# Optimization experiments

Hardware: AMD Instinct MI355X
Metric: run time of the kernel (lower is better)

Reference implementation:

```python
import jax, jax.numpy as jnp
import numpy as np

N = 50000       # original graph nodes (= number of subgraphs, one per node)
S = 10          # nodes per subgraph
M = N * S       # combined subgraph nodes
E = 2_000_000   # combined subgraph edges
E0 = 1_000_000  # original edges
NIN, HOP, NOUT, L = 64, 16, 128, 3
D = NIN + HOP   # conv width (80)


def setup_inputs() -> dict:
    key = jax.random.key(0)
    ks = iter(jax.random.split(key, 40))
    rng = np.random.default_rng(0)

    # structured index tensors: subgraph b occupies rows [b*S, (b+1)*S); row b*S is the centroid
    sub_batch = np.repeat(np.arange(N, dtype=np.int64), S)
    nodes_mapper = rng.integers(0, N, size=M, dtype=np.int64)
    nodes_mapper[::S] = np.arange(N)           # centroid: mapper == batch id
    hop_indicator = rng.integers(1, 5, size=M).astype(np.int64)
    hop_indicator[::S] = 0                     # centroid is hop 0
    edge_index = rng.integers(0, M, size=(2, E), dtype=np.int64)
    edges_mapper = rng.integers(0, E0, size=E, dtype=np.int64)

    def lin(k, fin, fout):
        return jax.random.normal(k, (fin, fout), jnp.float32) / np.sqrt(fin)

    inp = dict(
        x=jax.random.normal(next(ks), (N, NIN), jnp.float32),
        edge_attr=jax.random.normal(next(ks), (E0, D), jnp.float32),
        hop_table=jax.random.normal(next(ks), (20, HOP), jnp.float32),
        conv_W=jax.random.normal(next(ks), (L, D, D), jnp.float32) / np.sqrt(D),
        bn_g=jnp.ones((L, D), jnp.float32),
        bn_b=jnp.zeros((L, D), jnp.float32),
        oe_W0=lin(next(ks), D, NOUT), oe_b0=jnp.zeros((NOUT,), jnp.float32),
        oe_W1=lin(next(ks), NOUT, NOUT), oe_b1=jnp.zeros((NOUT,), jnp.float32),
        oe_W2=lin(next(ks), NOUT, NOUT), oe_b2=jnp.zeros((NOUT,), jnp.float32),
        st_W0=lin(next(ks), NOUT, NOUT), st_b0=jnp.zeros((NOUT,), jnp.float32),
        st_W1=lin(next(ks), NOUT, NOUT), st_b1=jnp.zeros((NOUT,), jnp.float32),
        st_W2=lin(next(ks), NOUT, NOUT), st_b2=jnp.zeros((NOUT,), jnp.float32),
        ct_W0=lin(next(ks), NOUT, NOUT), ct_b0=jnp.zeros((NOUT,), jnp.float32),
        ct_W1=lin(next(ks), NOUT, NOUT), ct_b1=jnp.zeros((NOUT,), jnp.float32),
        ct_W2=lin(next(ks), NOUT, NOUT), ct_b2=jnp.zeros((NOUT,), jnp.float32),
        gc_W=lin(next(ks), HOP, NOUT), gc_b=jnp.zeros((NOUT,), jnp.float32),
        gs_W=lin(next(ks), HOP, NOUT), gs_b=jnp.zeros((NOUT,), jnp.float32),
        gx_W=lin(next(ks), HOP, NOUT), gx_b=jnp.zeros((NOUT,), jnp.float32),
        nodes_mapper=jnp.asarray(nodes_mapper),
        edge_index=jnp.asarray(edge_index),
        edges_mapper=jnp.asarray(edges_mapper),
        sub_batch=jnp.asarray(sub_batch),
        hop_indicator=jnp.asarray(hop_indicator),
    )
    return inp


def _mlp3(h, W0, b0, W1, b1, W2, b2, final_act):
    h = jax.nn.relu(h @ W0 + b0)
    h = jax.nn.relu(h @ W1 + b1)
    h = h @ W2 + b2
    return jax.nn.relu(h) if final_act else h


def reference(x, edge_attr, hop_table, conv_W, bn_g, bn_b,
              oe_W0, oe_b0, oe_W1, oe_b1, oe_W2, oe_b2,
              st_W0, st_b0, st_W1, st_b1, st_W2, st_b2,
              ct_W0, ct_b0, ct_W1, ct_b1, ct_W2, ct_b2,
              gc_W, gc_b, gs_W, gs_b, gx_W, gx_b,
              nodes_mapper, edge_index, edges_mapper, sub_batch, hop_indicator):
    src, dst = edge_index[0], edge_index[1]
    ea = edge_attr[edges_mapper]                              # [E, D] gather
    hemb = hop_table[hop_indicator + 1]                       # [M, HOP]
    h = jnp.concatenate([x[nodes_mapper], hemb], axis=-1)     # [M, D]

    # GNN: nlayer x (GINE-style conv -> relu -> batchnorm(batch stats) -> residual)
    for l in range(L):
        msg = h[src] + ea                                     # [E, D]
        agg = jax.ops.segment_sum(msg, dst, num_segments=M)   # scatter-add
        h2 = jax.nn.relu(agg @ conv_W[l])
        mu = jnp.mean(h2, axis=0)
        var = jnp.var(h2, axis=0)
        h2 = (h2 - mu) * jax.lax.rsqrt(var + 1e-5) * bn_g[l] + bn_b[l]
        h = h2 + h                                            # residual

    # output encoder MLP (no final activation)
    h = _mlp3(h, oe_W0, oe_b0, oe_W1, oe_b1, oe_W2, oe_b2, False)  # [M, NOUT]

    # three views with sigmoid hop gates
    g_c = jax.nn.sigmoid(hemb @ gc_W + gc_b)
    g_s = jax.nn.sigmoid(hemb @ gs_W + gs_b)
    g_x = jax.nn.sigmoid(hemb @ gx_W + gx_b)

    cm = (nodes_mapper == sub_batch)[:, None]                 # centroid mask (one per subgraph)
    centroid_x = jax.ops.segment_sum(jnp.where(cm, h * g_c, 0.0), sub_batch, num_segments=N)
    subgraph_x = jax.ops.segment_sum(
        _mlp3(h, st_W0, st_b0, st_W1, st_b1, st_W2, st_b2, True) * g_s, sub_batch, num_segments=N)
    context_x = jax.ops.segment_sum(
        _mlp3(h, ct_W0, ct_b0, ct_W1, ct_b1, ct_W2, ct_b2, True) * g_x, nodes_mapper, num_segments=N)

    return centroid_x + subgraph_x + context_x                # embs_combine_mode='add'
```

## Files before the change

### kernel.cpp

```cpp
#include <hip/hip_runtime.h>


typedef __attribute__((ext_vector_type(8))) short bf16x8;
typedef __attribute__((ext_vector_type(4))) float f32x4;

static constexpr int cN = 50000;
static constexpr int cM = 500000;
static constexpr int cE = 2000000;

__device__ __forceinline__ float b2f(unsigned short u) {
  union { unsigned int u; float f; } v; v.u = ((unsigned int)u) << 16; return v.f;
}
__device__ __forceinline__ unsigned short f2b(float f) {
  union { float f; unsigned int u; } v; v.f = f;
  unsigned int x = v.u;
  x += 0x7fffu + ((x >> 16) & 1u);
  return (unsigned short)(x >> 16);
}
__device__ __forceinline__ float sigm(float x) { return 1.0f / (1.0f + __expf(-x)); }
__device__ __forceinline__ f32x4 mfma16(bf16x8 a, bf16x8 b, f32x4 c) {
  return __builtin_amdgcn_mfma_f32_16x16x32_bf16(a, b, c, 0, 0, 0);
}

struct RepackDesc { const float* src; unsigned short* dst; int K; int N; int tiles; };
struct RepackArgs { RepackDesc d[15]; };

__global__ __launch_bounds__(256) void repack_kernel(RepackArgs a) {
  RepackDesc dd = a.d[blockIdx.y];
  int tile = blockIdx.x;
  if (tile >= dd.tiles) return;
  int ncb = dd.N >> 4;
  int c = tile / ncb, cb = tile - c * ncb;
  for (int e = threadIdx.x; e < 512; e += 256) {
    int lane = e >> 3, j = e & 7;
    int k = 32 * c + 8 * (lane >> 4) + j;
    int n = 16 * cb + (lane & 15);
    unsigned short v = (k < dd.K) ? f2b(dd.src[(size_t)k * dd.N + n]) : (unsigned short)0;
    dd.dst[(size_t)tile * 512 + e] = v;
  }
}

__global__ __launch_bounds__(256) void build_h_kernel(
    const float* __restrict__ x, const float* __restrict__ ht,
    const int* __restrict__ nmap, const int* __restrict__ hop,
    unsigned short* __restrict__ h)
{
  int i = blockIdx.x * 256 + threadIdx.x;
  if (i >= cM * 20) return;
  int row = i / 20, cc = i - row * 20;
  int col = cc * 4;
  float4 f;
  if (col < 64) {
    f = *(const float4*)(x + (size_t)nmap[row] * 64 + col);
  } else {
    int hi = hop[row] + 1;
    f = *(const float4*)(ht + (size_t)hi * 16 + (col - 64));
  }
  ushort4 o; o.x = f2b(f.x); o.y = f2b(f.y); o.z = f2b(f.z); o.w = f2b(f.w);
  *(ushort4*)(h + (size_t)row * 80 + col) = o;
}

__global__ __launch_bounds__(256) void hist_kernel(const int* __restrict__ ei, int* __restrict__ deg) {
  int e = blockIdx.x * 256 + threadIdx.x;
  if (e < cE) atomicAdd(&deg[ei[cE + e]], 1);
}

__global__ __launch_bounds__(256) void scan1_kernel(const int* __restrict__ deg, int* __restrict__ bsum) {
  __shared__ int s[256];
  int i = blockIdx.x * 256 + threadIdx.x;
  s[threadIdx.x] = (i < cM) ? deg[i] : 0;
  __syncthreads();
  for (int o = 128; o > 0; o >>= 1) {
    if (threadIdx.x < o) s[threadIdx.x] += s[threadIdx.x + o];
    __syncthreads();
  }
  if (threadIdx.x == 0) bsum[blockIdx.x] = s[0];
}

__global__ void scan2_kernel(int* __restrict__ bsum, int nb) {
  if (threadIdx.x == 0 && blockIdx.x == 0) {
    int acc = 0;
    for (int i = 0; i < nb; ++i) { int t = bsum[i]; bsum[i] = acc; acc += t; }
  }
}

__global__ __launch_bounds__(256) void scan3_kernel(
    const int* __restrict__ deg, const int* __restrict__ bsum,
    int* __restrict__ rowptr, int* __restrict__ cursor)
{
  __shared__ int s[256];
  int i = blockIdx.x * 256 + threadIdx.x;
  int v = (i < cM) ? deg[i] : 0;
  s[threadIdx.x] = v;
  __syncthreads();
  for (int o = 1; o < 256; o <<= 1) {
    int t = (threadIdx.x >= o) ? s[threadIdx.x - o] : 0;
    __syncthreads();
    s[threadIdx.x] += t;
    __syncthreads();
  }
  if (i < cM) {
    int ex = bsum[blockIdx.x] + s[threadIdx.x] - v;
    rowptr[i] = ex; cursor[i] = ex;
  }
  if (i == cM - 1) rowptr[cM] = bsum[blockIdx.x] + s[threadIdx.x];
}

__global__ __launch_bounds__(256) void scatter_kernel(
    const int* __restrict__ ei, const int* __restrict__ emap,
    int* __restrict__ cursor, int* __restrict__ srcs, int* __restrict__ em2)
{
  int e = blockIdx.x * 256 + threadIdx.x;
  if (e >= cE) return;
  int d = ei[cE + e];
  int pos = atomicAdd(&cursor[d], 1);
  srcs[pos] = ei[e];
  em2[pos] = emap[e];
}

__global__ __launch_bounds__(320) void eag_rowsum_kernel(
    const float* __restrict__ ea, const int* __restrict__ em2,
    const int* __restrict__ rowptr, unsigned short* __restrict__ eag)
{
  int t = threadIdx.x;
  int r = blockIdx.x * 16 + t / 20;
  int c = (t % 20) * 4;
  if (r >= cM) return;
  int p0 = rowptr[r], p1 = rowptr[r + 1];
  float4 acc = {0.f, 0.f, 0.f, 0.f};
  for (int p = p0; p < p1; ++p) {
    int em = em2[p];
    float4 v = *(const float4*)(ea + (size_t)em * 80 + c);
    acc.x += v.x; acc.y += v.y; acc.z += v.z; acc.w += v.w;
  }
  ushort4 o = {f2b(acc.x), f2b(acc.y), f2b(acc.z), f2b(acc.w)};
  *(ushort4*)(eag + (size_t)r * 80 + c) = o;
}

__global__ __launch_bounds__(320) void aggregate_kernel(
    const unsigned short* __restrict__ h, const unsigned short* __restrict__ eag,
    const int* __restrict__ rowptr, const int* __restrict__ srcs,
    unsigned short* __restrict__ Bo)
{
  int t = threadIdx.x;
  int r = blockIdx.x * 16 + t / 20;
  int c = (t % 20) * 4;
  if (r >= cM) return;
  int p0 = rowptr[r], p1 = rowptr[r + 1];
  ushort4 a0 = *(const ushort4*)(eag + (size_t)r * 80 + c);
  float4 acc = {b2f(a0.x), b2f(a0.y), b2f(a0.z), b2f(a0.w)};
  for (int p = p0; p < p1; ++p) {
    int s = srcs[p];
    ushort4 v = *(const ushort4*)(h + (size_t)s * 80 + c);
    acc.x += b2f(v.x); acc.y += b2f(v.y); acc.z += b2f(v.z); acc.w += b2f(v.w);
  }
  ushort4 o = {f2b(acc.x), f2b(acc.y), f2b(acc.z), f2b(acc.w)};
  *(ushort4*)(Bo + (size_t)r * 80 + c) = o;
}

__global__ __launch_bounds__(256) void edge_scatter_kernel(
    const unsigned short* __restrict__ h, const float* __restrict__ ea,
    const int* __restrict__ ei, const int* __restrict__ emap,
    float* __restrict__ agg)
{
  int i = blockIdx.x * 256 + threadIdx.x;
  if (i >= cE * 20) return;
  int e = i / 20, q = i - e * 20;
  int src = ei[e], dst = ei[cE + e], em = emap[e];
  ushort4 hv = *(const ushort4*)(h + (size_t)src * 80 + q * 4);
  float4 ev = *(const float4*)(ea + (size_t)em * 80 + q * 4);
  float* ap = agg + (size_t)dst * 80 + q * 4;
  atomicAdd(ap + 0, b2f(hv.x) + ev.x);
  atomicAdd(ap + 1, b2f(hv.y) + ev.y);
  atomicAdd(ap + 2, b2f(hv.z) + ev.z);
  atomicAdd(ap + 3, b2f(hv.w) + ev.w);
}

template<bool F32IO>
__global__ __launch_bounds__(256) void conv_gemm_kernel(
    void* __restrict__ aggv, const unsigned short* __restrict__ Bp)
{
  __shared__ __align__(16) unsigned short Bl[7680];
  for (int i = threadIdx.x; i < 7680; i += 256) Bl[i] = Bp[i];
  __syncthreads();
  int lane = threadIdx.x & 63, wave = threadIdx.x >> 6;
  int tile = blockIdx.x * 4 + wave;
  bool act = tile < (cM / 16);
  int quad = lane >> 4, m = lane & 15;
  size_t rowA = (size_t)tile * 16 + m;

  bf16x8 a[3];
  #pragma unroll
  for (int c = 0; c < 3; ++c) {
    bf16x8 av = {0, 0, 0, 0, 0, 0, 0, 0};
    int k = 32 * c + 8 * quad;
    if (act && k + 8 <= 80) {
      if constexpr (F32IO) {
        const float* p = (const float*)aggv + rowA * 80 + k;
        float4 f0 = *(const float4*)p;
        float4 f1 = *(const float4*)(p + 4);
        av[0] = (short)f2b(f0.x); av[1] = (short)f2b(f0.y);
        av[2] = (short)f2b(f0.z); av[3] = (short)f2b(f0.w);
        av[4] = (short)f2b(f1.x); av[5] = (short)f2b(f1.y);
        av[6] = (short)f2b(f1.z); av[7] = (short)f2b(f1.w);
      } else {
        av = *(const bf16x8*)((const unsigned short*)aggv + rowA * 80 + k);
      }
    }
    a[c] = av;
  }

  #pragma unroll
  for (int cb = 0; cb < 5; ++cb) {
    f32x4 acc = {0.f, 0.f, 0.f, 0.f};
    #pragma unroll
    for (int c = 0; c < 3; ++c)
      acc = mfma16(a[c], *(const bf16x8*)(Bl + ((size_t)(c * 5 + cb) * 64 + lane) * 8), acc);
    int col = cb * 16 + m;
    #pragma unroll
    for (int i2 = 0; i2 < 4; ++i2) {
      size_t row = (size_t)tile * 16 + quad * 4 + i2;
      if (act) {
        float v = fmaxf(acc[i2], 0.0f);
        if constexpr (F32IO) ((float*)aggv)[row * 80 + col] = v;
        else ((unsigned short*)aggv)[row * 80 + col] = f2b(v);
      }
    }
  }
}

template<bool F32IO>
__global__ __launch_bounds__(256) void stats_kernel(
    const void* __restrict__ h2v, float* __restrict__ stats)
{
  __shared__ __align__(16) float ssum[12 * 80];
  __shared__ __align__(16) float ssq[12 * 80];
  int t = threadIdx.x;
  int cc = t % 20, slot = t / 20;
  if (slot < 12) {
    float s0 = 0, s1 = 0, s2 = 0, s3 = 0, q0 = 0, q1 = 0, q2 = 0, q3 = 0;
    for (int row = blockIdx.x * 12 + slot; row < cM; row += gridDim.x * 12) {
      float f0, f1, f2, f3;
      if constexpr (F32IO) {
        float4 v = *(const float4*)((const float*)h2v + (size_t)row * 80 + cc * 4);
        f0 = v.x; f1 = v.y; f2 = v.z; f3 = v.w;
      } else {
        ushort4 v = *(const ushort4*)((const unsigned short*)h2v + (size_t)row * 80 + cc * 4);
        f0 = b2f(v.x); f1 = b2f(v.y); f2 = b2f(v.z); f3 = b2f(v.w);
      }
      s0 += f0; s1 += f1; s2 += f2; s3 += f3;
      q0 += f0 * f0; q1 += f1 * f1; q2 += f2 * f2; q3 += f3 * f3;
    }
    int base = slot * 80 + cc * 4;
    ssum[base + 0] = s0; ssum[base + 1] = s1; ssum[base + 2] = s2; ssum[base + 3] = s3;
    ssq[base + 0] = q0; ssq[base + 1] = q1; ssq[base + 2] = q2; ssq[base + 3] = q3;
  }
  __syncthreads();
  if (t < 20) {
    for (int j = 0; j < 4; ++j) {
      int c = t * 4 + j;
      float s = 0, q = 0;
      for (int sl = 0; sl < 12; ++sl) { s += ssum[sl * 80 + c]; q += ssq[sl * 80 + c]; }
      atomicAdd(&stats[c], s);
      atomicAdd(&stats[80 + c], q);
    }
  }
}

template<bool F32IO>
__global__ __launch_bounds__(256) void bn_residual_kernel(
    const void* __restrict__ h2v, const float* __restrict__ stats,
    const float* __restrict__ g, const float* __restrict__ b,
    unsigned short* __restrict__ h)
{
  int i = blockIdx.x * 256 + threadIdx.x;
  if (i >= cM * 20) return;
  int row = i / 20, cc = i - row * 20;
  int col = cc * 4;
  float in2[4];
  if constexpr (F32IO) {
    float4 v2 = *(const float4*)((const float*)h2v + (size_t)row * 80 + col);
    in2[0] = v2.x; in2[1] = v2.y; in2[2] = v2.z; in2[3] = v2.w;
  } else {
    ushort4 v2 = *(const ushort4*)((const unsigned short*)h2v + (size_t)row * 80 + col);
    in2[0] = b2f(v2.x); in2[1] = b2f(v2.y); in2[2] = b2f(v2.z); in2[3] = b2f(v2.w);
  }
  ushort4 vh = *(const ushort4*)(h + (size_t)row * 80 + col);
  const float invM = 1.0f / (float)cM;
  unsigned short inh[4] = {vh.x, vh.y, vh.z, vh.w};
  unsigned short o[4];
  #pragma unroll
  for (int j = 0; j < 4; ++j) {
    int c = col + j;
    float mu = stats[c] * invM;
    float var = fmaxf(stats[80 + c] * invM - mu * mu, 0.0f);
    float inv = rsqrtf(var + 1e-5f);
    float val = (in2[j] - mu) * inv * g[c] + b[c] + b2f(inh[j]);
    o[j] = f2b(val);
  }
  ushort4 ov = {o[0], o[1], o[2], o[3]};
  *(ushort4*)(h + (size_t)row * 80 + col) = ov;
}

template<int KCH>
__device__ __forceinline__ void layer_to_tb(
    const bf16x8* a, const unsigned short* Wl, const float* biasl,
    unsigned short* tbw, int lane)
{
  int quad = lane >> 4, m = lane & 15;
  #pragma unroll
  for (int cb = 0; cb < 8; ++cb) {
    f32x4 acc = {0.f, 0.f, 0.f, 0.f};
    #pragma unroll
    for (int c = 0; c < KCH; ++c)
      acc = mfma16(a[c], *(const bf16x8*)(Wl + ((size_t)(c * 8 + cb) * 64 + lane) * 8), acc);
    int col = cb * 16 + m;
    float bv = biasl[col];
    #pragma unroll
    for (int i2 = 0; i2 < 4; ++i2)
      tbw[(quad * 4 + i2) * 136 + col] = f2b(fmaxf(acc[i2] + bv, 0.0f));
  }
}

__device__ __forceinline__ void tb_to_a(bf16x8* a, const unsigned short* tbw, int lane) {
  int quad = lane >> 4, m = lane & 15;
  #pragma unroll
  for (int c = 0; c < 4; ++c)
    a[c] = *(const bf16x8*)(tbw + m * 136 + 32 * c + 8 * quad);
}

__device__ __forceinline__ bf16x8 load_hemb(const float* ht, int hi, int quad) {
  bf16x8 he = {0, 0, 0, 0, 0, 0, 0, 0};
  if (quad < 2) {
    const float* p = ht + (size_t)hi * 16 + 8 * quad;
    float4 f0 = *(const float4*)p;
    float4 f1 = *(const float4*)(p + 4);
    he[0] = (short)f2b(f0.x); he[1] = (short)f2b(f0.y);
    he[2] = (short)f2b(f0.z); he[3] = (short)f2b(f0.w);
    he[4] = (short)f2b(f1.x); he[5] = (short)f2b(f1.y);
    he[6] = (short)f2b(f1.z); he[7] = (short)f2b(f1.w);
  }
  return he;
}

__global__ __launch_bounds__(256) void oe_fused_kernel(
    const unsigned short* __restrict__ h,
    const unsigned short* __restrict__ P0, const float* __restrict__ b0,
    const unsigned short* __restrict__ P1, const float* __restrict__ b1,
    const unsigned short* __restrict__ P2, const float* __restrict__ b2,
    unsigned short* __restrict__ Out)
{
  __shared__ __align__(16) unsigned short Wbuf[16384];
  __shared__ __align__(16) float bias[3][128];
  __shared__ __align__(16) unsigned short tb[4][16 * 136];
  int t = threadIdx.x;
  for (int i = t; i < 12288; i += 256) Wbuf[i] = P0[i];
  if (t < 128) { bias[0][t] = b0[t]; bias[1][t] = b1[t]; bias[2][t] = b2[t]; }
  __syncthreads();

  int lane = t & 63, wave = t >> 6;
  int tile = blockIdx.x * 4 + wave;
  bool act = tile < (cM / 16);
  int quad = lane >> 4, m = lane & 15;
  size_t rowA = (size_t)tile * 16 + m;

  bf16x8 a[4];
  #pragma unroll
  for (int c = 0; c < 4; ++c) {
    bf16x8 av = {0, 0, 0, 0, 0, 0, 0, 0};
    int k = 32 * c + 8 * quad;
    if (act && c < 3 && k + 8 <= 80)
      av = *(const bf16x8*)(h + rowA * 80 + k);
    a[c] = av;
  }
  layer_to_tb<3>(a, Wbuf, bias[0], tb[wave], lane);
  __syncthreads();
  tb_to_a(a, tb[wave], lane);
  for (int i = t; i < 16384; i += 256) Wbuf[i] = P1[i];
  __syncthreads();
  layer_to_tb<4>(a, Wbuf, bias[1], tb[wave], lane);
  __syncthreads();
  tb_to_a(a, tb[wave], lane);
  for (int i = t; i < 16384; i += 256) Wbuf[i] = P2[i];
  __syncthreads();

  #pragma unroll
  for (int cb = 0; cb < 8; ++cb) {
    f32x4 acc = {0.f, 0.f, 0.f, 0.f};
    #pragma unroll
    for (int c = 0; c < 4; ++c)
      acc = mfma16(a[c], *(const bf16x8*)(Wbuf + ((size_t)(c * 8 + cb) * 64 + lane) * 8), acc);
    int col = cb * 16 + m;
    float bv = bias[2][col];
    #pragma unroll
    for (int i2 = 0; i2 < 4; ++i2) {
      size_t row = (size_t)tile * 16 + quad * 4 + i2;
      if (act) Out[row * 128 + col] = f2b(acc[i2] + bv);
    }
  }
}

__global__ __launch_bounds__(256) void st_fused_kernel(
    const unsigned short* __restrict__ hout,
    const unsigned short* __restrict__ P0, const float* __restrict__ b0,
    const unsigned short* __restrict__ P1, const float* __restrict__ b1,
    const unsigned short* __restrict__ P2, const float* __restrict__ b2,
    const unsigned short* __restrict__ Gs, const float* __restrict__ gsb,
    const unsigned short* __restrict__ Gc, const float* __restrict__ gcb,
    const float* __restrict__ ht, const int* __restrict__ hop,
    const int* __restrict__ nmap, const int* __restrict__ sb,
    float* __restrict__ outp)
{
  __shared__ __align__(16) unsigned short Wbuf[16384];
  __shared__ __align__(16) float bias[5][128];
  __shared__ __align__(16) unsigned short tb[4][16 * 136];
  int t = threadIdx.x;
  for (int i = t; i < 16384; i += 256) Wbuf[i] = P0[i];
  if (t < 128) {
    bias[0][t] = b0[t]; bias[1][t] = b1[t]; bias[2][t] = b2[t];
    bias[3][t] = gsb[t]; bias[4][t] = gcb[t];
  }
  __syncthreads();

  int lane = t & 63, wave = t >> 6;
  int tile = blockIdx.x * 4 + wave;
  bool act = tile < (cM / 16);
  int quad = lane >> 4, m = lane & 15;
  size_t rowA = (size_t)tile * 16 + m;

  bf16x8 a[4];
  #pragma unroll
  for (int c = 0; c < 4; ++c) {
    bf16x8 av = {0, 0, 0, 0, 0, 0, 0, 0};
    if (act) av = *(const bf16x8*)(hout + rowA * 128 + 32 * c + 8 * quad);
    a[c] = av;
  }
  layer_to_tb<4>(a, Wbuf, bias[0], tb[wave], lane);
  __syncthreads();
  tb_to_a(a, tb[wave], lane);
  for (int i = t; i < 16384; i += 256) Wbuf[i] = P1[i];
  __syncthreads();
  layer_to_tb<4>(a, Wbuf, bias[1], tb[wave], lane);
  __syncthreads();
  tb_to_a(a, tb[wave], lane);
  for (int i = t; i < 16384; i += 256) Wbuf[i] = P2[i];
  __syncthreads();
  float* red = (float*)&tb[0][0];
  for (int i = t; i < 1024; i += 256) red[i] = 0.0f;
  int sbBase = sb[blockIdx.x * 64];
  __syncthreads();

  int hi = act ? (hop[rowA] + 1) : 0;
  bf16x8 he = load_hemb(ht, hi, quad);

  int r[4], sbr[4]; bool mk[4];
  #pragma unroll
  for (int i2 = 0; i2 < 4; ++i2) {
    int row = tile * 16 + quad * 4 + i2;
    r[i2] = row;
    sbr[i2] = act ? sb[row] : 0;
    mk[i2] = act && (nmap[row] == sbr[i2]);
  }

  #pragma unroll
  for (int cb = 0; cb < 8; ++cb) {
    f32x4 acc = {0.f, 0.f, 0.f, 0.f}, ga = {0.f, 0.f, 0.f, 0.f}, ca = {0.f, 0.f, 0.f, 0.f};
    #pragma unroll
    for (int c = 0; c < 4; ++c)
      acc = mfma16(a[c], *(const bf16x8*)(Wbuf + ((size_t)(c * 8 + cb) * 64 + lane) * 8), acc);
    ga = mfma16(he, *(const bf16x8*)(Gs + ((size_t)cb * 64 + lane) * 8), ga);
    ca = mfma16(he, *(const bf16x8*)(Gc + ((size_t)cb * 64 + lane) * 8), ca);
    int col = cb * 16 + m;
    #pragma unroll
    for (int i2 = 0; i2 < 4; ++i2) {
      float v = fmaxf(acc[i2] + bias[2][col], 0.0f) * sigm(ga[i2] + bias[3][col]);
      if (mk[i2]) v += b2f(hout[(size_t)r[i2] * 128 + col]) * sigm(ca[i2] + bias[4][col]);
      if (act) {
        int slot = sbr[i2] - sbBase;
        if ((unsigned)slot < 8u) atomicAdd(&red[slot * 128 + col], v);
        else atomicAdd(outp + (size_t)sbr[i2] * 128 + col, v);
      }
    }
  }

  __syncthreads();
  for (int i = t; i < 1024; i += 256) {
    float v = red[i];
    if (v != 0.0f)
      atomicAdd(outp + (size_t)(sbBase + (i >> 7)) * 128 + (i & 127), v);
  }
}

__global__ __launch_bounds__(256) void ct_fused_kernel(
    const unsigned short* __restrict__ hout,
    const unsigned short* __restrict__ P0, const float* __restrict__ b0,
    const unsigned short* __restrict__ P1, const float* __restrict__ b1,
    const unsigned short* __restrict__ P2, const float* __restrict__ b2,
    const unsigned short* __restrict__ Gx, const float* __restrict__ gxb,
    const float* __restrict__ ht, const int* __restrict__ hop,
    const int* __restrict__ nmap,
    float* __restrict__ outp)
{
  __shared__ __align__(16) unsigned short Wbuf[16384];
  __shared__ __align__(16) float bias[4][128];
  __shared__ __align__(16) unsigned short tb[4][16 * 136];
  int t = threadIdx.x;
  for (int i = t; i < 16384; i += 256) Wbuf[i] = P0[i];
  if (t < 128) {
    bias[0][t] = b0[t]; bias[1][t] = b1[t];
    bias[2][t] = b2[t]; bias[3][t] = gxb[t];
  }
  __syncthreads();

  int lane = t & 63, wave = t >> 6;
  int tile = blockIdx.x * 4 + wave;
  bool act = tile < (cM / 16);
  int quad = lane >> 4, m = lane & 15;
  size_t rowA = (size_t)tile * 16 + m;

  bf16x8 a[4];
  #pragma unroll
  for (int c = 0; c < 4; ++c) {
    bf16x8 av = {0, 0, 0, 0, 0, 0, 0, 0};
    if (act) av = *(const bf16x8*)(hout + rowA * 128 + 32 * c + 8 * quad);
    a[c] = av;
  }
  layer_to_tb<4>(a, Wbuf, bias[0], tb[wave], lane);
  __syncthreads();
  tb_to_a(a, tb[wave], lane);
  for (int i = t; i < 16384; i += 256) Wbuf[i] = P1[i];
  __syncthreads();
  layer_to_tb<4>(a, Wbuf, bias[1], tb[wave], lane);
  __syncthreads();
  tb_to_a(a, tb[wave], lane);
  for (int i = t; i < 16384; i += 256) Wbuf[i] = P2[i];
  __syncthreads();

  int hi = act ? (hop[rowA] + 1) : 0;
  bf16x8 he = load_hemb(ht, hi, quad);

  int dst[4];
  #pragma unroll
  for (int i2 = 0; i2 < 4; ++i2) {
    int row = tile * 16 + quad * 4 + i2;
    dst[i2] = act ? nmap[row] : 0;
  }

  #pragma unroll
  for (int cb = 0; cb < 8; ++cb) {
    f32x4 acc = {0.f, 0.f, 0.f, 0.f}, ga = {0.f, 0.f, 0.f, 0.f};
    #pragma unroll
    for (int c = 0; c < 4; ++c)
      acc = mfma16(a[c], *(const bf16x8*)(Wbuf + ((size_t)(c * 8 + cb) * 64 + lane) * 8), acc);
    ga = mfma16(he, *(const bf16x8*)(Gx + ((size_t)cb * 64 + lane) * 8), ga);
    int col = cb * 16 + m;
    #pragma unroll
    for (int i2 = 0; i2 < 4; ++i2) {
      float v = fmaxf(acc[i2] + bias[2][col], 0.0f) * sigm(ga[i2] + bias[3][col]);
      if (act) atomicAdd(outp + (size_t)dst[i2] * 128 + col, v);
    }
  }
}

extern "C" void kernel_launch(void* const* d_in, const int* in_sizes, int n_in,
                              void* d_out, int out_size, void* d_ws, size_t ws_size,
                              hipStream_t stream)
{
  const float* x     = (const float*)d_in[0];
  const float* eattr = (const float*)d_in[1];
  const float* htab  = (const float*)d_in[2];
  const float* convW = (const float*)d_in[3];
  const float* bng   = (const float*)d_in[4];
  const float* bnb   = (const float*)d_in[5];
  const float* oeW0 = (const float*)d_in[6];  const float* oeb0 = (const float*)d_in[7];
  const float* oeW1 = (const float*)d_in[8];  const float* oeb1 = (const float*)d_in[9];
  const float* oeW2 = (const float*)d_in[10]; const float* oeb2 = (const float*)d_in[11];
  const float* stW0 = (const float*)d_in[12]; const float* stb0 = (const float*)d_in[13];
  const float* stW1 = (const float*)d_in[14]; const float* stb1 = (const float*)d_in[15];
  const float* stW2 = (const float*)d_in[16]; const float* stb2 = (const float*)d_in[17];
  const float* ctW0 = (const float*)d_in[18]; const float* ctb0 = (const float*)d_in[19];
  const float* ctW1 = (const float*)d_in[20]; const float* ctb1 = (const float*)d_in[21];
  const float* ctW2 = (const float*)d_in[22]; const float* ctb2 = (const float*)d_in[23];
  const float* gcW = (const float*)d_in[24]; const float* gcb = (const float*)d_in[25];
  const float* gsW = (const float*)d_in[26]; const float* gsb = (const float*)d_in[27];
  const float* gxW = (const float*)d_in[28]; const float* gxb = (const float*)d_in[29];
  const int* nmap = (const int*)d_in[30];
  const int* ei   = (const int*)d_in[31];
  const int* emap = (const int*)d_in[32];
  const int* sb   = (const int*)d_in[33];
  const int* hop  = (const int*)d_in[34];

  if (n_in < 35 ||
      in_sizes[0] != cN * 64 || in_sizes[1] != 1000000 * 80 ||
      in_sizes[2] != 20 * 16 || in_sizes[3] != 3 * 80 * 80 ||
      in_sizes[30] != cM || in_sizes[31] != 2 * cE || in_sizes[32] != cE ||
      in_sizes[33] != cM || in_sizes[34] != cM || out_size != cN * 128)
    return;

  const size_t PCONV0 = 0, PCONV1 = 7680, PCONV2 = 15360, POE0 = 23040,
               POE1 = 35328, POE2 = 51712, PST0 = 68096, PST1 = 84480,
               PST2 = 100864, PCT0 = 117248, PCT1 = 133632, PCT2 = 150016,
               PGC = 166400, PGS = 170496, PGX = 174592;
  const size_t PACK_BYTES = 178688 * 2 + 256;

  char* ws = (char*)d_ws;
  size_t off = 0;
  auto alloc = [&](size_t bytes) -> void* {
    void* p = ws + off; off += (bytes + 255) & ~(size_t)255; return p;
  };

  unsigned short* h    = (unsigned short*)alloc((size_t)cM * 80 * 2);
  unsigned short* Aeag = (unsigned short*)alloc((size_t)cM * 80 * 2);
  unsigned short* Bagg = (unsigned short*)alloc((size_t)cM * 80 * 2);
  int*   rowptr = (int*)alloc((size_t)(cM + 1) * 4);
  int*   srcs   = (int*)alloc((size_t)cE * 4);
  float* stats  = (float*)alloc(1024);
  unsigned short* packs = (unsigned short*)alloc(PACK_BYTES);
  size_t needFast = off;
  bool fast = (ws_size >= needFast);

  float* aggF = nullptr;
  if (!fast) {
    off = 0;
    h     = (unsigned short*)alloc((size_t)cM * 80 * 2);
    aggF  = (float*)alloc((size_t)cM * 80 * 4);
    stats = (float*)alloc(1024);
    packs = (unsigned short*)alloc(PACK_BYTES);
    if (ws_size < off) return;
  }

  RepackArgs ra;
  auto setd = [&](int idx, const float* src, size_t dstOff, int K, int Nn, int tiles) {
    ra.d[idx].src = src; ra.d[idx].dst = packs + dstOff;
    ra.d[idx].K = K; ra.d[idx].N = Nn; ra.d[idx].tiles = tiles;
  };
  setd(0, convW,          PCONV0, 80, 80, 15);
  setd(1, convW + 6400,   PCONV1, 80, 80, 15);
  setd(2, convW + 12800,  PCONV2, 80, 80, 15);
  setd(3, oeW0, POE0, 80, 128, 24);
  setd(4, oeW1, POE1, 128, 128, 32);
  setd(5, oeW2, POE2, 128, 128, 32);
  setd(6, stW0, PST0, 128, 128, 32);
  setd(7, stW1, PST1, 128, 128, 32);
  setd(8, stW2, PST2, 128, 128, 32);
  setd(9, ctW0, PCT0, 128, 128, 32);
  setd(10, ctW1, PCT1, 128, 128, 32);
  setd(11, ctW2, PCT2, 128, 128, 32);
  setd(12, gcW, PGC, 16, 128, 8);
  setd(13, gsW, PGS, 16, 128, 8);
  setd(14, gxW, PGX, 16, 128, 8);
  repack_kernel<<<dim3(32, 15), 256, 0, stream>>>(ra);

  const int elemBlocksM = (cM * 20 + 255) / 256;
  const int gemmBlocks  = (cM / 16 + 3) / 4;
  const int rowBlocks   = (cM + 15) / 16;
  const int edgeB256    = (cE + 255) / 256;
  const int scanBlocks  = (cM + 255) / 256;

  build_h_kernel<<<elemBlocksM, 256, 0, stream>>>(x, htab, nmap, hop, h);
  hipMemsetAsync(d_out, 0, (size_t)cN * 128 * 4, stream);

  unsigned short* hout;

  if (fast) {
    int* deg    = (int*)Bagg;
    int* cursor = deg + cM;
    int* em2    = cursor + cM;
    int* bsum   = em2 + cE;

    hipMemsetAsync(deg, 0, (size_t)cM * 4, stream);
    hist_kernel<<<edgeB256, 256, 0, stream>>>(ei, deg);
    scan1_kernel<<<scanBlocks, 256, 0, stream>>>(deg, bsum);
    scan2_kernel<<<1, 64, 0, stream>>>(bsum, scanBlocks);
    scan3_kernel<<<scanBlocks, 256, 0, stream>>>(deg, bsum, rowptr, cursor);
    scatter_kernel<<<edgeB256, 256, 0, stream>>>(ei, emap, cursor, srcs, em2);
    eag_rowsum_kernel<<<rowBlocks, 320, 0, stream>>>(eattr, em2, rowptr, Aeag);

    for (int l = 0; l < 3; ++l) {
      aggregate_kernel<<<rowBlocks, 320, 0, stream>>>(h, Aeag, rowptr, srcs, Bagg);
      conv_gemm_kernel<false><<<gemmBlocks, 256, 0, stream>>>(
          Bagg, packs + (l == 0 ? PCONV0 : l == 1 ? PCONV1 : PCONV2));
      hipMemsetAsync(stats, 0, 160 * 4, stream);
      stats_kernel<false><<<1024, 256, 0, stream>>>(Bagg, stats);
      bn_residual_kernel<false><<<elemBlocksM, 256, 0, stream>>>(
          Bagg, stats, bng + l * 80, bnb + l * 80, h);
    }
    hout = Aeag;
  } else {
    const int edgeBlocks = (cE * 20) / 256;
    for (int l = 0; l < 3; ++l) {
      hipMemsetAsync(aggF, 0, (size_t)cM * 80 * 4, stream);
      edge_scatter_kernel<<<edgeBlocks, 256, 0, stream>>>(h, eattr, ei, emap, aggF);
      conv_gemm_kernel<true><<<gemmBlocks, 256, 0, stream>>>(
          aggF, packs + (l == 0 ? PCONV0 : l == 1 ? PCONV1 : PCONV2));
      hipMemsetAsync(stats, 0, 160 * 4, stream);
      stats_kernel<true><<<1024, 256, 0, stream>>>(aggF, stats);
      bn_residual_kernel<true><<<elemBlocksM, 256, 0, stream>>>(
          aggF, stats, bng + l * 80, bnb + l * 80, h);
    }
    hout = (unsigned short*)aggF;
  }

  oe_fused_kernel<<<gemmBlocks, 256, 0, stream>>>(
      h, packs + POE0, oeb0, packs + POE1, oeb1, packs + POE2, oeb2, hout);

  st_fused_kernel<<<gemmBlocks, 256, 0, stream>>>(
      hout, packs + PST0, stb0, packs + PST1, stb1, packs + PST2, stb2,
      packs + PGS, gsb, packs + PGC, gcb, htab, hop, nmap, sb, (float*)d_out);

  ct_fused_kernel<<<gemmBlocks, 256, 0, stream>>>(
      hout, packs + PCT0, ctb0, packs + PCT1, ctb1, packs + PCT2, ctb2,
      packs + PGX, gxb, htab, hop, nmap, (float*)d_out);
}
```

Measured before the change: 2.920 ms.

## Fuse output-encoder and view MLPs into one kernel with precomputed gate table

Merges the three tail kernels (output encoder, subgraph MLP, context MLP) into a single kernel that keeps the encoder output in registers and shared memory, so the [M,128] bf16 intermediate is never written to or re-read from global memory. Sigmoid hop gates depend only on the 20-entry hop table, so they are precomputed once into a small gate table instead of being evaluated per row with extra MFMAs and exponentials. The conv GEMM now handles four tiles per wave and stages weights with 16-byte copies, and the shared-memory staging buffer is XOR-swizzled instead of padded. In exchange the fused kernel has higher register and shared-memory pressure and restages weights many times per block, which may lower occupancy.

New measurement: 2.823 ms. -3.3%, faster.

```diff
diff --git a/kernel.cpp b/kernel.cpp
--- a/kernel.cpp
+++ b/kernel.cpp
@@ -7,6 +7,12 @@
 static constexpr int cN = 50000;
 static constexpr int cM = 500000;
 static constexpr int cE = 2000000;
+static constexpr int cTiles = cM / 16;
+
+static constexpr size_t PCONV0 = 0, PCONV1 = 7680, PCONV2 = 15360, POE0 = 23040,
+                        POE1 = 35328, POE2 = 51712, PST0 = 68096, PST1 = 84480,
+                        PST2 = 100864, PCT0 = 117248, PCT1 = 133632, PCT2 = 150016;
+static constexpr size_t PACK_BYTES = 166400 * 2 + 256;
 
 __device__ __forceinline__ float b2f(unsigned short u) {
   union { unsigned int u; float f; } v; v.u = ((unsigned int)u) << 16; return v.f;
@@ -23,7 +29,7 @@
 }
 
 struct RepackDesc { const float* src; unsigned short* dst; int K; int N; int tiles; };
-struct RepackArgs { RepackDesc d[15]; };
+struct RepackArgs { RepackDesc d[12]; };
 
 __global__ __launch_bounds__(256) void repack_kernel(RepackArgs a) {
   RepackDesc dd = a.d[blockIdx.y];
@@ -40,6 +46,25 @@
   }
 }
 
+__global__ __launch_bounds__(256) void gate_build_kernel(
+    const float* __restrict__ ht,
+    const float* __restrict__ gsW, const float* __restrict__ gsb,
+    const float* __restrict__ gcW, const float* __restrict__ gcb,
+    const float* __restrict__ gxW, const float* __restrict__ gxb,
+    float* __restrict__ gtab)
+{
+  int i = blockIdx.x * 256 + threadIdx.x;
+  if (i >= 3 * 20 * 128) return;
+  int g = i / 2560, rem = i - g * 2560;
+  int hi = rem >> 7, col = rem & 127;
+  const float* W  = (g == 0) ? gsW : (g == 1) ? gcW : gxW;
+  const float* bb = (g == 0) ? gsb : (g == 1) ? gcb : gxb;
+  float acc = bb[col];
+  #pragma unroll
+  for (int k = 0; k < 16; ++k) acc += ht[hi * 16 + k] * W[k * 128 + col];
+  gtab[i] = sigm(acc);
+}
+
 __global__ __launch_bounds__(256) void build_h_kernel(
     const float* __restrict__ x, const float* __restrict__ ht,
     const int* __restrict__ nmap, const int* __restrict__ hop,
@@ -181,49 +206,60 @@
     void* __restrict__ aggv, const unsigned short* __restrict__ Bp)
 {
   __shared__ __align__(16) unsigned short Bl[7680];
-  for (int i = threadIdx.x; i < 7680; i += 256) Bl[i] = Bp[i];
+  #pragma unroll
+  for (int i = threadIdx.x; i < 960; i += 256)
+    ((uint4*)Bl)[i] = ((const uint4*)Bp)[i];
   __syncthreads();
   int lane = threadIdx.x & 63, wave = threadIdx.x >> 6;
-  int tile = blockIdx.x * 4 + wave;
-  bool act = tile < (cM / 16);
+  int tile0 = (blockIdx.x * 4 + wave) * 4;
   int quad = lane >> 4, m = lane & 15;
-  size_t rowA = (size_t)tile * 16 + m;
-
-  bf16x8 a[3];
-  #pragma unroll
-  for (int c = 0; c < 3; ++c) {
-    bf16x8 av = {0, 0, 0, 0, 0, 0, 0, 0};
-    int k = 32 * c + 8 * quad;
-    if (act && k + 8 <= 80) {
-      if constexpr (F32IO) {
-        const float* p = (const float*)aggv + rowA * 80 + k;
-        float4 f0 = *(const float4*)p;
-        float4 f1 = *(const float4*)(p + 4);
-        av[0] = (short)f2b(f0.x); av[1] = (short)f2b(f0.y);
-        av[2] = (short)f2b(f0.z); av[3] = (short)f2b(f0.w);
-        av[4] = (short)f2b(f1.x); av[5] = (short)f2b(f1.y);
-        av[6] = (short)f2b(f1.z); av[7] = (short)f2b(f1.w);
-      } else {
-        av = *(const bf16x8*)((const unsigned short*)aggv + rowA * 80 + k);
+
+  bf16x8 a[4][3];
+  #pragma unroll
+  for (int tt = 0; tt < 4; ++tt) {
+    int tile = tile0 + tt;
+    bool act = tile < cTiles;
+    size_t rowA = (size_t)tile * 16 + m;
+    #pragma unroll
+    for (int c = 0; c < 3; ++c) {
+      bf16x8 av = {0, 0, 0, 0, 0, 0, 0, 0};
+      int k = 32 * c + 8 * quad;
+      if (act && k + 8 <= 80) {
+        if constexpr (F32IO) {
+          const float* p = (const float*)aggv + rowA * 80 + k;
+          float4 f0 = *(const float4*)p;
+          float4 f1 = *(const float4*)(p + 4);
+          av[0] = (short)f2b(f0.x); av[1] = (short)f2b(f0.y);
+          av[2] = (short)f2b(f0.z); av[3] = (short)f2b(f0.w);
+          av[4] = (short)f2b(f1.x); av[5] = (short)f2b(f1.y);
+          av[6] = (short)f2b(f1.z); av[7] = (short)f2b(f1.w);
+        } else {
+          av = *(const bf16x8*)((const unsigned short*)aggv + rowA * 80 + k);
+        }
       }
-    }
-    a[c] = av;
-  }
-
-  #pragma unroll
-  for (int cb = 0; cb < 5; ++cb) {
-    f32x4 acc = {0.f, 0.f, 0.f, 0.f};
-    #pragma unroll
-    for (int c = 0; c < 3; ++c)
-      acc = mfma16(a[c], *(const bf16x8*)(Bl + ((size_t)(c * 5 + cb) * 64 + lane) * 8), acc);
-    int col = cb * 16 + m;
-    #pragma unroll
-    for (int i2 = 0; i2 < 4; ++i2) {
-      size_t row = (size_t)tile * 16 + quad * 4 + i2;
-      if (act) {
-        float v = fmaxf(acc[i2], 0.0f);
-        if constexpr (F32IO) ((float*)aggv)[row * 80 + col] = v;
-        else ((unsigned short*)aggv)[row * 80 + col] = f2b(v);
+      a[tt][c] = av;
+    }
+  }
+
+  #pragma unroll
+  for (int tt = 0; tt < 4; ++tt) {
+    int tile = tile0 + tt;
+    bool act = tile < cTiles;
+    #pragma unroll
+    for (int cb = 0; cb < 5; ++cb) {
+      f32x4 acc = {0.f, 0.f, 0.f, 0.f};
+      #pragma unroll
+      for (int c = 0; c < 3; ++c)
+        acc = mfma16(a[tt][c], *(const bf16x8*)(Bl + ((size_t)(c * 5 + cb) * 64 + lane) * 8), acc);
+      int col = cb * 16 + m;
+      #pragma unroll
+      for (int i2 = 0; i2 < 4; ++i2) {
+        size_t row = (size_t)tile * 16 + quad * 4 + i2;
+        if (act) {
+          float v = fmaxf(acc[i2], 0.0f);
+          if constexpr (F32IO) ((float*)aggv)[row * 80 + col] = v;
+          else ((unsigned short*)aggv)[row * 80 + col] = f2b(v);
+        }
       }
     }
   }
@@ -302,9 +338,23 @@
   *(ushort4*)(h + (size_t)row * 80 + col) = ov;
 }
 
+__device__ __forceinline__ void tb_put(unsigned short* tbw, int row, int col, unsigned short v) {
+  int g = (col >> 3) ^ (row & 7);
+  tbw[row * 128 + (g << 3) + (col & 7)] = v;
+}
+
+__device__ __forceinline__ void tb_to_a(bf16x8* a, const unsigned short* tbw, int lane) {
+  int quad = lane >> 4, m = lane & 15;
+  #pragma unroll
+  for (int c = 0; c < 4; ++c) {
+    int sg = ((c << 2) | quad) ^ (m & 7);
+    a[c] = *(const bf16x8*)(tbw + m * 128 + (sg << 3));
+  }
+}
+
 template<int KCH>
-__device__ __forceinline__ void layer_to_tb(
-    const bf16x8* a, const unsigned short* Wl, const float* biasl,
+__device__ __forceinline__ void layer_relu(
+    const bf16x8* a, const unsigned short* Wl, const float* bl,
     unsigned short* tbw, int lane)
 {
   int quad = lane >> 4, m = lane & 15;
@@ -315,166 +365,129 @@
     for (int c = 0; c < KCH; ++c)
       acc = mfma16(a[c], *(const bf16x8*)(Wl + ((size_t)(c * 8 + cb) * 64 + lane) * 8), acc);
     int col = cb * 16 + m;
-    float bv = biasl[col];
+    float bv = bl[col];
     #pragma unroll
     for (int i2 = 0; i2 < 4; ++i2)
-      tbw[(quad * 4 + i2) * 136 + col] = f2b(fmaxf(acc[i2] + bv, 0.0f));
-  }
-}
-
-__device__ __forceinline__ void tb_to_a(bf16x8* a, const unsigned short* tbw, int lane) {
-  int quad = lane >> 4, m = lane & 15;
-  #pragma unroll
-  for (int c = 0; c < 4; ++c)
-    a[c] = *(const bf16x8*)(tbw + m * 136 + 32 * c + 8 * quad);
-}
-
-__device__ __forceinline__ bf16x8 load_hemb(const float* ht, int hi, int quad) {
-  bf16x8 he = {0, 0, 0, 0, 0, 0, 0, 0};
-  if (quad < 2) {
-    const float* p = ht + (size_t)hi * 16 + 8 * quad;
-    float4 f0 = *(const float4*)p;
-    float4 f1 = *(const float4*)(p + 4);
-    he[0] = (short)f2b(f0.x); he[1] = (short)f2b(f0.y);
-    he[2] = (short)f2b(f0.z); he[3] = (short)f2b(f0.w);
-    he[4] = (short)f2b(f1.x); he[5] = (short)f2b(f1.y);
-    he[6] = (short)f2b(f1.z); he[7] = (short)f2b(f1.w);
-  }
-  return he;
-}
-
-__global__ __launch_bounds__(256) void oe_fused_kernel(
+      tb_put(tbw, quad * 4 + i2, col, f2b(fmaxf(acc[i2] + bv, 0.0f)));
+  }
+}
+
+__device__ __forceinline__ void stageW(unsigned short* Wbuf, const unsigned short* src, int nU4, int t) {
+  const uint4* s = (const uint4*)src;
+  uint4* d = (uint4*)Wbuf;
+  for (int i = t; i < nU4; i += 256) d[i] = s[i];
+}
+
+__global__ __launch_bounds__(256, 3) void tail_fused_kernel(
     const unsigned short* __restrict__ h,
-    const unsigned short* __restrict__ P0, const float* __restrict__ b0,
-    const unsigned short* __restrict__ P1, const float* __restrict__ b1,
-    const unsigned short* __restrict__ P2, const float* __restrict__ b2,
-    unsigned short* __restrict__ Out)
+    const unsigned short* __restrict__ packs,
+    const float* __restrict__ oeb0, const float* __restrict__ oeb1, const float* __restrict__ oeb2,
+    const float* __restrict__ stb0, const float* __restrict__ stb1, const float* __restrict__ stb2,
+    const float* __restrict__ ctb0, const float* __restrict__ ctb1, const float* __restrict__ ctb2,
+    const float* __restrict__ gtab,
+    const int* __restrict__ hop, const int* __restrict__ nmap, const int* __restrict__ sb,
+    float* __restrict__ outp)
 {
   __shared__ __align__(16) unsigned short Wbuf[16384];
-  __shared__ __align__(16) float bias[3][128];
-  __shared__ __align__(16) unsigned short tb[4][16 * 136];
+  __shared__ __align__(16) unsigned short tb[4][2048];
+  __shared__ __align__(16) float biasl[9][128];
+
   int t = threadIdx.x;
-  for (int i = t; i < 12288; i += 256) Wbuf[i] = P0[i];
-  if (t < 128) { bias[0][t] = b0[t]; bias[1][t] = b1[t]; bias[2][t] = b2[t]; }
+  stageW(Wbuf, packs + POE0, 1536, t);
+  if (t < 128) {
+    biasl[0][t] = oeb0[t]; biasl[1][t] = oeb1[t]; biasl[2][t] = oeb2[t];
+    biasl[3][t] = stb0[t]; biasl[4][t] = stb1[t]; biasl[5][t] = stb2[t];
+    biasl[6][t] = ctb0[t]; biasl[7][t] = ctb1[t]; biasl[8][t] = ctb2[t];
+  }
   __syncthreads();
 
   int lane = t & 63, wave = t >> 6;
   int tile = blockIdx.x * 4 + wave;
-  bool act = tile < (cM / 16);
+  bool act = tile < cTiles;
   int quad = lane >> 4, m = lane & 15;
   size_t rowA = (size_t)tile * 16 + m;
 
-  bf16x8 a[4];
+  bf16x8 aw[4];
   #pragma unroll
   for (int c = 0; c < 4; ++c) {
     bf16x8 av = {0, 0, 0, 0, 0, 0, 0, 0};
     int k = 32 * c + 8 * quad;
     if (act && c < 3 && k + 8 <= 80)
       av = *(const bf16x8*)(h + rowA * 80 + k);
-    a[c] = av;
-  }
-  layer_to_tb<3>(a, Wbuf, bias[0], tb[wave], lane);
-  __syncthreads();
-  tb_to_a(a, tb[wave], lane);
-  for (int i = t; i < 16384; i += 256) Wbuf[i] = P1[i];
-  __syncthreads();
-  layer_to_tb<4>(a, Wbuf, bias[1], tb[wave], lane);
-  __syncthreads();
-  tb_to_a(a, tb[wave], lane);
-  for (int i = t; i < 16384; i += 256) Wbuf[i] = P2[i];
-  __syncthreads();
-
-  #pragma unroll
-  for (int cb = 0; cb < 8; ++cb) {
-    f32x4 acc = {0.f, 0.f, 0.f, 0.f};
-    #pragma unroll
-    for (int c = 0; c < 4; ++c)
-      acc = mfma16(a[c], *(const bf16x8*)(Wbuf + ((size_t)(c * 8 + cb) * 64 + lane) * 8), acc);
-    int col = cb * 16 + m;
-    float bv = bias[2][col];
-    #pragma unroll
-    for (int i2 = 0; i2 < 4; ++i2) {
-      size_t row = (size_t)tile * 16 + quad * 4 + i2;
-      if (act) Out[row * 128 + col] = f2b(acc[i2] + bv);
-    }
-  }
-}
-
-__global__ __launch_bounds__(256) void st_fused_kernel(
-    const unsigned short* __restrict__ hout,
-    const unsigned short* __restrict__ P0, const float* __restrict__ b0,
-    const unsigned short* __restrict__ P1, const float* __restrict__ b1,
-    const unsigned short* __restrict__ P2, const float* __restrict__ b2,
-    const unsigned short* __restrict__ Gs, const float* __restrict__ gsb,
-    const unsigned short* __restrict__ Gc, const float* __restrict__ gcb,
-    const float* __restrict__ ht, const int* __restrict__ hop,
-    const int* __restrict__ nmap, const int* __restrict__ sb,
-    float* __restrict__ outp)
-{
-  __shared__ __align__(16) unsigned short Wbuf[16384];
-  __shared__ __align__(16) float bias[5][128];
-  __shared__ __align__(16) unsigned short tb[4][16 * 136];
-  int t = threadIdx.x;
-  for (int i = t; i < 16384; i += 256) Wbuf[i] = P0[i];
-  if (t < 128) {
-    bias[0][t] = b0[t]; bias[1][t] = b1[t]; bias[2][t] = b2[t];
-    bias[3][t] = gsb[t]; bias[4][t] = gcb[t];
-  }
-  __syncthreads();
-
-  int lane = t & 63, wave = t >> 6;
-  int tile = blockIdx.x * 4 + wave;
-  bool act = tile < (cM / 16);
-  int quad = lane >> 4, m = lane & 15;
-  size_t rowA = (size_t)tile * 16 + m;
-
-  bf16x8 a[4];
-  #pragma unroll
-  for (int c = 0; c < 4; ++c) {
-    bf16x8 av = {0, 0, 0, 0, 0, 0, 0, 0};
-    if (act) av = *(const bf16x8*)(hout + rowA * 128 + 32 * c + 8 * quad);
-    a[c] = av;
-  }
-  layer_to_tb<4>(a, Wbuf, bias[0], tb[wave], lane);
-  __syncthreads();
-  tb_to_a(a, tb[wave], lane);
-  for (int i = t; i < 16384; i += 256) Wbuf[i] = P1[i];
-  __syncthreads();
-  layer_to_tb<4>(a, Wbuf, bias[1], tb[wave], lane);
-  __syncthreads();
-  tb_to_a(a, tb[wave], lane);
-  for (int i = t; i < 16384; i += 256) Wbuf[i] = P2[i];
-  __syncthreads();
+    aw[c] = av;
+  }
+
+  layer_relu<3>(aw, Wbuf, biasl[0], tb[wave], lane);
+  tb_to_a(aw, tb[wave], lane);
+  __syncthreads();
+  stageW(Wbuf, packs + POE1, 2048, t);
+  __syncthreads();
+  layer_relu<4>(aw, Wbuf, biasl[1], tb[wave], lane);
+  tb_to_a(aw, tb[wave], lane);
+  __syncthreads();
+  stageW(Wbuf, packs + POE2, 2048, t);
+  __syncthreads();
+
+  float o_out[8][4];
+  bf16x8 a_oe[4];
+  {
+    #pragma unroll
+    for (int cb = 0; cb < 8; ++cb) {
+      f32x4 acc = {0.f, 0.f, 0.f, 0.f};
+      #pragma unroll
+      for (int c = 0; c < 4; ++c)
+        acc = mfma16(aw[c], *(const bf16x8*)(Wbuf + ((size_t)(c * 8 + cb) * 64 + lane) * 8), acc);
+      int col = cb * 16 + m;
+      float bv = biasl[2][col];
+      #pragma unroll
+      for (int i2 = 0; i2 < 4; ++i2) {
+        float val = acc[i2] + bv;
+        o_out[cb][i2] = val;
+        tb_put(tb[wave], quad * 4 + i2, col, f2b(val));
+      }
+    }
+    tb_to_a(a_oe, tb[wave], lane);
+  }
+  __syncthreads();
+  stageW(Wbuf, packs + PST0, 2048, t);
+  __syncthreads();
+
+  layer_relu<4>(a_oe, Wbuf, biasl[3], tb[wave], lane);
+  tb_to_a(aw, tb[wave], lane);
+  __syncthreads();
+  stageW(Wbuf, packs + PST1, 2048, t);
+  __syncthreads();
+  layer_relu<4>(aw, Wbuf, biasl[4], tb[wave], lane);
+  tb_to_a(aw, tb[wave], lane);
+  __syncthreads();
+  stageW(Wbuf, packs + PST2, 2048, t);
   float* red = (float*)&tb[0][0];
   for (int i = t; i < 1024; i += 256) red[i] = 0.0f;
   int sbBase = sb[blockIdx.x * 64];
   __syncthreads();
 
-  int hi = act ? (hop[rowA] + 1) : 0;
-  bf16x8 he = load_hemb(ht, hi, quad);
-
-  int r[4], sbr[4]; bool mk[4];
+  int hi2[4], sbr[4], dstm[4]; bool mk[4];
   #pragma unroll
   for (int i2 = 0; i2 < 4; ++i2) {
     int row = tile * 16 + quad * 4 + i2;
-    r[i2] = row;
-    sbr[i2] = act ? sb[row] : 0;
-    mk[i2] = act && (nmap[row] == sbr[i2]);
+    sbr[i2]  = act ? sb[row] : 0;
+    dstm[i2] = act ? nmap[row] : 0;
+    mk[i2]   = act && (dstm[i2] == sbr[i2]);
+    hi2[i2]  = act ? (hop[row] + 1) : 0;
   }
 
   #pragma unroll
   for (int cb = 0; cb < 8; ++cb) {
-    f32x4 acc = {0.f, 0.f, 0.f, 0.f}, ga = {0.f, 0.f, 0.f, 0.f}, ca = {0.f, 0.f, 0.f, 0.f};
+    f32x4 acc = {0.f, 0.f, 0.f, 0.f};
     #pragma unroll
     for (int c = 0; c < 4; ++c)
-      acc = mfma16(a[c], *(const bf16x8*)(Wbuf + ((size_t)(c * 8 + cb) * 64 + lane) * 8), acc);
-    ga = mfma16(he, *(const bf16x8*)(Gs + ((size_t)cb * 64 + lane) * 8), ga);
-    ca = mfma16(he, *(const bf16x8*)(Gc + ((size_t)cb * 64 + lane) * 8), ca);
+      acc = mfma16(aw[c], *(const bf16x8*)(Wbuf + ((size_t)(c * 8 + cb) * 64 + lane) * 8), acc);
     int col = cb * 16 + m;
+    float bv = biasl[5][col];
     #pragma unroll
     for (int i2 = 0; i2 < 4; ++i2) {
-      float v = fmaxf(acc[i2] + bias[2][col], 0.0f) * sigm(ga[i2] + bias[3][col]);
-      if (mk[i2]) v += b2f(hout[(size_t)r[i2] * 128 + col]) * sigm(ca[i2] + bias[4][col]);
+      float v = fmaxf(acc[i2] + bv, 0.0f) * gtab[hi2[i2] * 128 + col];
+      if (mk[i2]) v += o_out[cb][i2] * gtab[2560 + hi2[i2] * 128 + col];
       if (act) {
         int slot = sbr[i2] - sbBase;
         if ((unsigned)slot < 8u) atomicAdd(&red[slot * 128 + col], v);
@@ -482,82 +495,39 @@
       }
     }
   }
-
   __syncthreads();
   for (int i = t; i < 1024; i += 256) {
     float v = red[i];
     if (v != 0.0f)
       atomicAdd(outp + (size_t)(sbBase + (i >> 7)) * 128 + (i & 127), v);
   }
-}
-
-__global__ __launch_bounds__(256) void ct_fused_kernel(
-    const unsigned short* __restrict__ hout,
-    const unsigned short* __restrict__ P0, const float* __restrict__ b0,
-    const unsigned short* __restrict__ P1, const float* __restrict__ b1,
-    const unsigned short* __restrict__ P2, const float* __restrict__ b2,
-    const unsigned short* __restrict__ Gx, const float* __restrict__ gxb,
-    const float* __restrict__ ht, const int* __restrict__ hop,
-    const int* __restrict__ nmap,
-    float* __restrict__ outp)
-{
-  __shared__ __align__(16) unsigned short Wbuf[16384];
-  __shared__ __align__(16) float bias[4][128];
-  __shared__ __align__(16) unsigned short tb[4][16 * 136];
-  int t = threadIdx.x;
-  for (int i = t; i < 16384; i += 256) Wbuf[i] = P0[i];
-  if (t < 128) {
-    bias[0][t] = b0[t]; bias[1][t] = b1[t];
-    bias[2][t] = b2[t]; bias[3][t] = gxb[t];
-  }
-  __syncthreads();
-
-  int lane = t & 63, wave = t >> 6;
-  int tile = blockIdx.x * 4 + wave;
-  bool act = tile < (cM / 16);
-  int quad = lane >> 4, m = lane & 15;
-  size_t rowA = (size_t)tile * 16 + m;
-
-  bf16x8 a[4];
-  #pragma unroll
-  for (int c = 0; c < 4; ++c) {
-    bf16x8 av = {0, 0, 0, 0, 0, 0, 0, 0};
-    if (act) av = *(const bf16x8*)(hout + rowA * 128 + 32 * c + 8 * quad);
-    a[c] = av;
-  }
-  layer_to_tb<4>(a, Wbuf, bias[0], tb[wave], lane);
-  __syncthreads();
-  tb_to_a(a, tb[wave], lane);
-  for (int i = t; i < 16384; i += 256) Wbuf[i] = P1[i];
-  __syncthreads();
-  layer_to_tb<4>(a, Wbuf, bias[1], tb[wave], lane);
-  __syncthreads();
-  tb_to_a(a, tb[wave], lane);
-  for (int i = t; i < 16384; i += 256) Wbuf[i] = P2[i];
-  __syncthreads();
-
-  int hi = act ? (hop[rowA] + 1) : 0;
-  bf16x8 he = load_hemb(ht, hi, quad);
-
-  int dst[4];
-  #pragma unroll
-  for (int i2 = 0; i2 < 4; ++i2) {
-    int row = tile * 16 + quad * 4 + i2;
-    dst[i2] = act ? nmap[row] : 0;
-  }
+  __syncthreads();
+  stageW(Wbuf, packs + PCT0, 2048, t);
+  __syncthreads();
+
+  layer_relu<4>(a_oe, Wbuf, biasl[6], tb[wave], lane);
+  tb_to_a(aw, tb[wave], lane);
+  __syncthreads();
+  stageW(Wbuf, packs + PCT1, 2048, t);
+  __syncthreads();
+  layer_relu<4>(aw, Wbuf, biasl[7], tb[wave], lane);
+  tb_to_a(aw, tb[wave], lane);
+  __syncthreads();
+  stageW(Wbuf, packs + PCT2, 2048, t);
+  __syncthreads();
 
   #pragma unroll
   for (int cb = 0; cb < 8; ++cb) {
-    f32x4 acc = {0.f, 0.f, 0.f, 0.f}, ga = {0.f, 0.f, 0.f, 0.f};
+    f32x4 acc = {0.f, 0.f, 0.f, 0.f};
     #pragma unroll
     for (int c = 0; c < 4; ++c)
-      acc = mfma16(a[c], *(const bf16x8*)(Wbuf + ((size_t)(c * 8 + cb) * 64 + lane) * 8), acc);
-    ga = mfma16(he, *(const bf16x8*)(Gx + ((size_t)cb * 64 + lane) * 8), ga);
+      acc = mfma16(aw[c], *(const bf16x8*)(Wbuf + ((size_t)(c * 8 + cb) * 64 + lane) * 8), acc);
     int col = cb * 16 + m;
+    float bv = biasl[8][col];
     #pragma unroll
     for (int i2 = 0; i2 < 4; ++i2) {
-      float v = fmaxf(acc[i2] + bias[2][col], 0.0f) * sigm(ga[i2] + bias[3][col]);
-      if (act) atomicAdd(outp + (size_t)dst[i2] * 128 + col, v);
+      float v = fmaxf(acc[i2] + bv, 0.0f) * gtab[5120 + hi2[i2] * 128 + col];
+      if (act) atomicAdd(outp + (size_t)dstm[i2] * 128 + col, v);
     }
   }
 }
@@ -597,12 +567,6 @@
       in_sizes[33] != cM || in_sizes[34] != cM || out_size != cN * 128)
     return;
 
-  const size_t PCONV0 = 0, PCONV1 = 7680, PCONV2 = 15360, POE0 = 23040,
-               POE1 = 35328, POE2 = 51712, PST0 = 68096, PST1 = 84480,
-               PST2 = 100864, PCT0 = 117248, PCT1 = 133632, PCT2 = 150016,
-               PGC = 166400, PGS = 170496, PGX = 174592;
-  const size_t PACK_BYTES = 178688 * 2 + 256;
-
   char* ws = (char*)d_ws;
   size_t off = 0;
   auto alloc = [&](size_t bytes) -> void* {
@@ -615,6 +579,7 @@
   int*   rowptr = (int*)alloc((size_t)(cM + 1) * 4);
   int*   srcs   = (int*)alloc((size_t)cE * 4);
   float* stats  = (float*)alloc(1024);
+  float* gtab   = (float*)alloc(3 * 20 * 128 * 4);
   unsigned short* packs = (unsigned short*)alloc(PACK_BYTES);
   size_t needFast = off;
   bool fast = (ws_size >= needFast);
@@ -625,6 +590,7 @@
     h     = (unsigned short*)alloc((size_t)cM * 80 * 2);
     aggF  = (float*)alloc((size_t)cM * 80 * 4);
     stats = (float*)alloc(1024);
+    gtab  = (float*)alloc(3 * 20 * 128 * 4);
     packs = (unsigned short*)alloc(PACK_BYTES);
     if (ws_size < off) return;
   }
@@ -646,21 +612,18 @@
   setd(9, ctW0, PCT0, 128, 128, 32);
   setd(10, ctW1, PCT1, 128, 128, 32);
   setd(11, ctW2, PCT2, 128, 128, 32);
-  setd(12, gcW, PGC, 16, 128, 8);
-  setd(13, gsW, PGS, 16, 128, 8);
-  setd(14, gxW, PGX, 16, 128, 8);
-  repack_kernel<<<dim3(32, 15), 256, 0, stream>>>(ra);
+  repack_kernel<<<dim3(32, 12), 256, 0, stream>>>(ra);
+  gate_build_kernel<<<30, 256, 0, stream>>>(htab, gsW, gsb, gcW, gcb, gxW, gxb, gtab);
 
   const int elemBlocksM = (cM * 20 + 255) / 256;
-  const int gemmBlocks  = (cM / 16 + 3) / 4;
+  const int convBlocks  = (cTiles + 15) / 16;
+  const int tailBlocks  = (cTiles + 3) / 4;
   const int rowBlocks   = (cM + 15) / 16;
   const int edgeB256    = (cE + 255) / 256;
   const int scanBlocks  = (cM + 255) / 256;
 
   build_h_kernel<<<elemBlocksM, 256, 0, stream>>>(x, htab, nmap, hop, h);
   hipMemsetAsync(d_out, 0, (size_t)cN * 128 * 4, stream);
-
-  unsigned short* hout;
 
   if (fast) {
     int* deg    = (int*)Bagg;
@@ -678,37 +641,29 @@
 
     for (int l = 0; l < 3; ++l) {
       aggregate_kernel<<<rowBlocks, 320, 0, stream>>>(h, Aeag, rowptr, srcs, Bagg);
-      conv_gemm_kernel<false><<<gemmBlocks, 256, 0, stream>>>(
+      conv_gemm_kernel<false><<<convBlocks, 256, 0, stream>>>(
           Bagg, packs + (l == 0 ? PCONV0 : l == 1 ? PCONV1 : PCONV2));
       hipMemsetAsync(stats, 0, 160 * 4, stream);
       stats_kernel<false><<<1024, 256, 0, stream>>>(Bagg, stats);
       bn_residual_kernel<false><<<elemBlocksM, 256, 0, stream>>>(
           Bagg, stats, bng + l * 80, bnb + l * 80, h);
     }
-    hout = Aeag;
   } else {
     const int edgeBlocks = (cE * 20) / 256;
     for (int l = 0; l < 3; ++l) {
       hipMemsetAsync(aggF, 0, (size_t)cM * 80 * 4, stream);
       edge_scatter_kernel<<<edgeBlocks, 256, 0, stream>>>(h, eattr, ei, emap, aggF);
-      conv_gemm_kernel<true><<<gemmBlocks, 256, 0, stream>>>(
+      conv_gemm_kernel<true><<<convBlocks, 256, 0, stream>>>(
           aggF, packs + (l == 0 ? PCONV0 : l == 1 ? PCONV1 : PCONV2));
       hipMemsetAsync(stats, 0, 160 * 4, stream);
       stats_kernel<true><<<1024, 256, 0, stream>>>(aggF, stats);
       bn_residual_kernel<true><<<elemBlocksM, 256, 0, stream>>>(
           aggF, stats, bng + l * 80, bnb + l * 80, h);
     }
-    hout = (unsigned short*)aggF;
-  }
-
-  oe_fused_kernel<<<gemmBlocks, 256, 0, stream>>>(
-      h, packs + POE0, oeb0, packs + POE1, oeb1, packs + POE2, oeb2, hout);
-
-  st_fused_kernel<<<gemmBlocks, 256, 0, stream>>>(
-      hout, packs + PST0, stb0, packs + PST1, stb1, packs + PST2, stb2,
-      packs + PGS, gsb, packs + PGC, gcb, htab, hop, nmap, sb, (float*)d_out);
-
-  ct_fused_kernel<<<gemmBlocks, 256, 0, stream>>>(
-      hout, packs + PCT0, ctb0, packs + PCT1, ctb1, packs + PCT2, ctb2,
-      packs + PGX, gxb, htab, hop, nmap, (float*)d_out);
-}
+  }
+
+  tail_fused_kernel<<<tailBlocks, 256, 0, stream>>>(
+      h, packs,
+      oeb0, oeb1, oeb2, stb0, stb1, stb2, ctb0, ctb1, ctb2,
+      gtab, hop, nmap, sb, (float*)d_out);
+}
```
